# Kernel tuning notes

Measured on AMD Instinct MI355X. Metric: run time of the kernel, lower is better.

## Reference

```python
import jax, jax.numpy as jnp
import numpy as np

B = 8192      # batch
C = 4096      # in_channels
K = 5         # group_size (odd, centered window)


def setup_inputs() -> dict:
    key = jax.random.key(0)
    kx, kw, kb = jax.random.split(key, 3)
    x = jax.random.normal(kx, (B, C), dtype=jnp.float32)
    # Banded weights: W[i, k] multiplies x[:, i + k - K//2] (zero outside range).
    W = jax.random.normal(kw, (C, K), dtype=jnp.float32) * 0.1
    b = jax.random.normal(kb, (C,), dtype=jnp.float32) * 0.1
    return {"x": x, "W": W, "b": b}


def reference(x, W, b):
    # out[:, i] = sum_k W[i, k] * x[:, i + k - K//2] + b[i]
    # Boundary clipping in the original == zero padding here.
    Bn, Cn = x.shape
    Kn = W.shape[1]
    half = Kn // 2
    xp = jnp.pad(x, ((0, 0), (half, half)))  # [B, C + K - 1]
    acc = jnp.zeros_like(x)
    for k in range(Kn):  # tiny fixed loop (K=5), fused shift-multiply-add
        acc = acc + xp[:, k:k + Cn] * W[:, k]
    return acc + b
```

## Files before the change

kernel.cpp:

```cpp
#include <hip/hip_runtime.h>


#define B_ROWS 8192
#define C_CH   4096
#define KWIN   5
#define ROWS_PER_BLOCK 8

typedef float vf4 __attribute__((ext_vector_type(4)));

__global__ __launch_bounds__(256, 8) void grouped_linear_kernel(
    const float* __restrict__ x, const float* __restrict__ W,
    const float* __restrict__ bias, float* __restrict__ out)
{
    const int chunk = (blockIdx.x << 8) + threadIdx.x;
    const int c     = chunk << 2;
    const int r0    = blockIdx.y * ROWS_PER_BLOCK;

    const float4* W4 = (const float4*)(W + (size_t)c * KWIN);
    const float4 w0 = W4[0];
    const float4 w1 = W4[1];
    const float4 w2 = W4[2];
    const float4 w3 = W4[3];
    const float4 w4 = W4[4];
    const float4 bv = ((const float4*)bias)[chunk];

    const bool has_m = (c > 0);
    const bool has_p = (c + 4 < C_CH);
    const float4 zero = make_float4(0.f, 0.f, 0.f, 0.f);

    const float4* xrow = (const float4*)(x   + (size_t)r0 * C_CH);
    float4*       orow = (float4*)      (out + (size_t)r0 * C_CH);
    const int rstride = C_CH / 4;

    float4 xm = has_m ? xrow[chunk - 1] : zero;
    float4 xc = xrow[chunk];
    float4 xp = has_p ? xrow[chunk + 1] : zero;

    #pragma unroll
    for (int r = 0; r < ROWS_PER_BLOCK; ++r) {
        float4 nm = zero, nc = zero, np = zero;
        if (r + 1 < ROWS_PER_BLOCK) {
            const float4* nx = xrow + rstride;
            nm = has_m ? nx[chunk - 1] : zero;
            nc = nx[chunk];
            np = has_p ? nx[chunk + 1] : zero;
        }

        const float win0 = xm.z, win1 = xm.w;
        const float win2 = xc.x, win3 = xc.y, win4 = xc.z, win5 = xc.w;
        const float win6 = xp.x, win7 = xp.y;

        float4 o;
        o.x = fmaf(w0.x, win0, fmaf(w0.y, win1, fmaf(w0.z, win2, fmaf(w0.w, win3, fmaf(w1.x, win4, bv.x)))));
        o.y = fmaf(w1.y, win1, fmaf(w1.z, win2, fmaf(w1.w, win3, fmaf(w2.x, win4, fmaf(w2.y, win5, bv.y)))));
        o.z = fmaf(w2.z, win2, fmaf(w2.w, win3, fmaf(w3.x, win4, fmaf(w3.y, win5, fmaf(w3.z, win6, bv.z)))));
        o.w = fmaf(w3.w, win3, fmaf(w4.x, win4, fmaf(w4.y, win5, fmaf(w4.z, win6, fmaf(w4.w, win7, bv.w)))));

        vf4 ov; ov.x = o.x; ov.y = o.y; ov.z = o.z; ov.w = o.w;
        __builtin_nontemporal_store(ov, (vf4*)(orow + chunk));

        xm = nm; xc = nc; xp = np;
        xrow += rstride;
        orow += rstride;
    }
}

extern "C" void kernel_launch(void* const* d_in, const int* in_sizes, int n_in,
                              void* d_out, int out_size, void* d_ws, size_t ws_size,
                              hipStream_t stream) {
    const float* x    = (const float*)d_in[0];
    const float* W    = (const float*)d_in[1];
    const float* bias = (const float*)d_in[2];
    float* out = (float*)d_out;

    dim3 grid(C_CH / 4 / 256, B_ROWS / ROWS_PER_BLOCK);
    dim3 block(256);
    grouped_linear_kernel<<<grid, block, 0, stream>>>(x, W, bias, out);
}
```

Measured before the change: 241.0 us.

## Exchange neighbor halo via wavefront shuffles and use plain stores

Instead of each thread loading its left and right neighbor float4 chunks from global memory, threads now load only their own chunk and obtain neighbor values through cross-lane shuffles. Only the edge lanes of each 64-wide wavefront issue an extra halo load. This cuts redundant global and cache load traffic by roughly two thirds per row. It adds shuffle instructions and lane-conditional selects, and replaces the nontemporal output stores with ordinary stores, which may change cache behavior for the write stream.

```diff
diff --git a/kernel.cpp b/kernel.cpp
--- a/kernel.cpp
+++ b/kernel.cpp
@@ -5,8 +5,7 @@
 #define C_CH   4096
 #define KWIN   5
 #define ROWS_PER_BLOCK 8
-
-typedef float vf4 __attribute__((ext_vector_type(4)));
+#define NCHUNK (C_CH / 4)
 
 __global__ __launch_bounds__(256, 8) void grouped_linear_kernel(
     const float* __restrict__ x, const float* __restrict__ W,
@@ -15,6 +14,7 @@
     const int chunk = (blockIdx.x << 8) + threadIdx.x;
     const int c     = chunk << 2;
     const int r0    = blockIdx.y * ROWS_PER_BLOCK;
+    const int lane  = threadIdx.x & 63;
 
     const float4* W4 = (const float4*)(W + (size_t)c * KWIN);
     const float4 w0 = W4[0];
@@ -24,31 +24,40 @@
     const float4 w4 = W4[4];
     const float4 bv = ((const float4*)bias)[chunk];
 
-    const bool has_m = (c > 0);
-    const bool has_p = (c + 4 < C_CH);
     const float4 zero = make_float4(0.f, 0.f, 0.f, 0.f);
+
+    const bool is_lo = (lane == 0);
+    const bool is_hi = (lane == 63);
+    const int  hchunk = is_lo ? (chunk - 1) : (chunk + 1);
+    const bool hvalid = (is_lo && chunk > 0) || (is_hi && chunk + 1 < NCHUNK);
 
     const float4* xrow = (const float4*)(x   + (size_t)r0 * C_CH);
     float4*       orow = (float4*)      (out + (size_t)r0 * C_CH);
     const int rstride = C_CH / 4;
 
-    float4 xm = has_m ? xrow[chunk - 1] : zero;
     float4 xc = xrow[chunk];
-    float4 xp = has_p ? xrow[chunk + 1] : zero;
+    float4 hl = zero;
+    if (hvalid) hl = xrow[hchunk];
 
     #pragma unroll
     for (int r = 0; r < ROWS_PER_BLOCK; ++r) {
-        float4 nm = zero, nc = zero, np = zero;
+        float4 nc = zero, nh = zero;
         if (r + 1 < ROWS_PER_BLOCK) {
             const float4* nx = xrow + rstride;
-            nm = has_m ? nx[chunk - 1] : zero;
             nc = nx[chunk];
-            np = has_p ? nx[chunk + 1] : zero;
+            if (hvalid) nh = nx[hchunk];
         }
 
-        const float win0 = xm.z, win1 = xm.w;
+        float mz = __shfl_up(xc.z, 1);
+        float mw = __shfl_up(xc.w, 1);
+        float px = __shfl_down(xc.x, 1);
+        float py = __shfl_down(xc.y, 1);
+
+        const float win0 = is_lo ? hl.z : mz;
+        const float win1 = is_lo ? hl.w : mw;
         const float win2 = xc.x, win3 = xc.y, win4 = xc.z, win5 = xc.w;
-        const float win6 = xp.x, win7 = xp.y;
+        const float win6 = is_hi ? hl.x : px;
+        const float win7 = is_hi ? hl.y : py;
 
         float4 o;
         o.x = fmaf(w0.x, win0, fmaf(w0.y, win1, fmaf(w0.z, win2, fmaf(w0.w, win3, fmaf(w1.x, win4, bv.x)))));
@@ -56,10 +65,9 @@
         o.z = fmaf(w2.z, win2, fmaf(w2.w, win3, fmaf(w3.x, win4, fmaf(w3.y, win5, fmaf(w3.z, win6, bv.z)))));
         o.w = fmaf(w3.w, win3, fmaf(w4.x, win4, fmaf(w4.y, win5, fmaf(w4.z, win6, fmaf(w4.w, win7, bv.w)))));
 
-        vf4 ov; ov.x = o.x; ov.y = o.y; ov.z = o.z; ov.w = o.w;
-        __builtin_nontemporal_store(ov, (vf4*)(orow + chunk));
+        orow[chunk] = o;
 
-        xm = nm; xc = nc; xp = np;
+        xc = nc; hl = nh;
         xrow += rstride;
         orow += rstride;
     }
```

After: 237.8 us. Within noise of the previous version (-1.3%).
